# Kernel tuning notes

Hardware: AMD Instinct MI355X
Metric: run time of the kernel (lower is better)

The kernel has to match this reference:

```python
import jax, jax.numpy as jnp
import numpy as np

B, H, N, D = 4, 16, 2048, 64

def setup_inputs() -> dict:
    key = jax.random.key(0)
    kq, kk, kv = jax.random.split(key, 3)
    q = jax.random.normal(kq, (B, H, N, D), dtype=jnp.float32)
    k = jax.random.normal(kk, (B, H, N, D), dtype=jnp.float32)
    v = jax.random.normal(kv, (B, H, N, D), dtype=jnp.float32)
    return {"q": q, "k": k, "v": v}

def reference(q, k, v):
    head_dim = q.shape[-1]
    scale = 1.0 / jnp.sqrt(jnp.asarray(head_dim, dtype=q.dtype))
    # scores: [B, H, N, N]
    attn = jnp.einsum('bhqd,bhkd->bhqk', q, k) * scale
    attn = jax.nn.softmax(attn, axis=-1)
    # output: [B, H, N, D]
    return jnp.einsum('bhqk,bhkd->bhqd', attn, v)
```

## Files before the change

### kernel.cpp

```cpp
#include <hip/hip_runtime.h>
#include <hip/hip_bf16.h>
#include <math.h>

#define NBATCH 4
#define NHEAD 16
#define NSEQ 2048
#define DHEAD 64
#define QBLK 128
#define KVBLK 64
#define NTILE (NSEQ / KVBLK)
#define NHTOT (NBATCH * NHEAD)
#define KV_TILE_BYTES 16384
#define KVB_BYTES ((size_t)NHTOT * NTILE * (size_t)KV_TILE_BYTES)
#define WS_NEED KVB_BYTES
#define QSCALE (0.125f * 1.4426950408889634f)

typedef __attribute__((ext_vector_type(8))) short bf16x8;
typedef __attribute__((ext_vector_type(4))) short short4v;
typedef __attribute__((ext_vector_type(16))) float f32x16;

union BF8U { unsigned u[4]; bf16x8 v; };

__device__ __forceinline__ unsigned short f2bf(float f) {
  unsigned u = __float_as_uint(f);
  u = (u + 0x7FFFu + ((u >> 16) & 1u)) >> 16;
  return (unsigned short)u;
}
__device__ __forceinline__ unsigned pack2(float a, float b) {
  return (unsigned)f2bf(a) | ((unsigned)f2bf(b) << 16);
}
__device__ __forceinline__ unsigned cvtpk(float a, float b) {
  unsigned r;
  asm("v_cvt_pk_bf16_f32 %0, %1, %2" : "=v"(r) : "v"(a), "v"(b));
  return r;
}
__device__ __forceinline__ float exp2_fast(float x) {
#if __has_builtin(__builtin_amdgcn_exp2f)
  return __builtin_amdgcn_exp2f(x);
#else
  return __expf(x * 0.69314718055994531f);
#endif
}
__device__ __forceinline__ void gload_lds16(const void* g, void* l) {
  __builtin_amdgcn_global_load_lds(
      (const __attribute__((address_space(1))) void*)g,
      (__attribute__((address_space(3))) void*)l, 16, 0, 0);
}

__global__ __launch_bounds__(256) void prep_kernel(
    const float* __restrict__ K, const float* __restrict__ V,
    char* __restrict__ KVb) {
  __shared__ float vsm[64][68];
  const int t = threadIdx.x;
  const int hb = blockIdx.x;
  const int head = hb >> 5;
  const int tile = hb & 31;
  const float* kp = K + ((size_t)head * NSEQ + tile * KVBLK) * DHEAD;
  const float* vp = V + ((size_t)head * NSEQ + tile * KVBLK) * DHEAD;
  char* out = KVb + (size_t)hb * KV_TILE_BYTES;
#pragma unroll
  for (int j = 0; j < 2; ++j) {
    const int n = t + j * 256;
    const int key = n >> 3, ch = (n >> 1) & 3, hi = n & 1;
    const int d0 = ch * 16 + hi * 8;
    const float4 f0 = *(const float4*)(kp + key * DHEAD + d0);
    const float4 f1 = *(const float4*)(kp + key * DHEAD + d0 + 4);
    BF8U u;
    u.u[0] = cvtpk(f0.x, f0.y); u.u[1] = cvtpk(f0.z, f0.w);
    u.u[2] = cvtpk(f1.x, f1.y); u.u[3] = cvtpk(f1.z, f1.w);
    const int kk = key & 31;
    const int m2 = (kk >> 2) ^ ((kk & 3) << 1);
    const int off = ((key >> 5) << 12) | ((kk & 3) << 10) | (hi << 9) | (ch << 7) | (m2 << 4);
    *(bf16x8*)(out + off) = u.v;
  }
#pragma unroll
  for (int p = 0; p < 4; ++p) {
    const int key = (t & 15) + 16 * p;
    const int d0 = (t >> 4) * 4;
    *(float4*)(&vsm[key][d0]) = *(const float4*)(vp + key * DHEAD + d0);
  }
  __syncthreads();
#pragma unroll
  for (int j = 0; j < 2; ++j) {
    const int s = t + j * 256;
    const int aa = (s >> 4) & 3;
    const int sl = s & 7;
    const int d5 = ((sl ^ ((aa & 1) << 2)) << 2) | aa;
    const int khi = (s >> 3) & 1;
    const int c2 = (s >> 6) & 7;
    const int ch = c2 >> 1, dblk = c2 & 1;
    const int d = dblk * 32 + d5;
    const int k0 = ch * 16 + khi * 8;
    BF8U u;
    u.u[0] = cvtpk(vsm[k0 + 0][d], vsm[k0 + 1][d]);
    u.u[1] = cvtpk(vsm[k0 + 2][d], vsm[k0 + 3][d]);
    u.u[2] = cvtpk(vsm[k0 + 4][d], vsm[k0 + 5][d]);
    u.u[3] = cvtpk(vsm[k0 + 6][d], vsm[k0 + 7][d]);
    *(bf16x8*)(out + 8192 + (s << 4)) = u.v;
  }
}

__global__ __launch_bounds__(256, 3) void fattn_kernel(
    const float* __restrict__ Q, const char* __restrict__ KVb,
    float* __restrict__ O) {
  __shared__ __align__(128) char smem[4][8192];

  const int tid = threadIdx.x;
  const int l = tid & 63;
  const int wv = tid >> 6;
  const int l31 = l & 31;
  const int HL = l >> 5;

  const int head = blockIdx.x;
  const int q0 = blockIdx.y * QBLK + wv * 32;
  const size_t base = (size_t)head * NSEQ * DHEAD;

  bf16x8 qf[4];
  {
    const float* qrow = Q + base + (size_t)(q0 + l31) * DHEAD + HL * 8;
#pragma unroll
    for (int ch = 0; ch < 4; ++ch) {
      const float4 f0 = *(const float4*)(qrow + ch * 16);
      const float4 f1 = *(const float4*)(qrow + ch * 16 + 4);
      BF8U u;
      u.u[0] = cvtpk(f0.x * QSCALE, f0.y * QSCALE);
      u.u[1] = cvtpk(f0.z * QSCALE, f0.w * QSCALE);
      u.u[2] = cvtpk(f1.x * QSCALE, f1.y * QSCALE);
      u.u[3] = cvtpk(f1.z * QSCALE, f1.w * QSCALE);
      qf[ch] = u.v;
    }
  }

  const int kk = l31;
  const int m2x = (kk >> 2) ^ ((kk & 3) << 1);
  const int kread = ((kk & 3) << 10) + (HL << 9) + (m2x << 4);
  const int vsl = (l31 >> 2) ^ ((l & 1) << 2);
  const int vread = ((l & 3) << 8) + (HL << 7) + (vsl << 4);

  const char* tb = KVb + (size_t)head * NTILE * KV_TILE_BYTES;
  char* kb0 = smem[0]; char* kb1 = smem[1];
  char* vb0 = smem[2]; char* vb1 = smem[3];

#define STAGE_K(T, DST)                                                     \
  { const char* s_ = tb + (size_t)(T) * KV_TILE_BYTES;                      \
    gload_lds16(s_ + ((wv << 1) + 0) * 1024 + l * 16, (DST) + ((wv << 1) + 0) * 1024); \
    gload_lds16(s_ + ((wv << 1) + 1) * 1024 + l * 16, (DST) + ((wv << 1) + 1) * 1024); }
#define STAGE_V(T, DST)                                                     \
  { const char* s_ = tb + (size_t)(T) * KV_TILE_BYTES + 8192;               \
    gload_lds16(s_ + ((wv << 1) + 0) * 1024 + l * 16, (DST) + ((wv << 1) + 0) * 1024); \
    gload_lds16(s_ + ((wv << 1) + 1) * 1024 + l * 16, (DST) + ((wv << 1) + 1) * 1024); }

#define QK_MFMA(KB, D0, D1)                                                 \
  { const char* kbp_ = (const char*)(KB);                                   \
    { const bf16x8 ka0 = *(const bf16x8*)(kbp_ + kread);                    \
      const bf16x8 ka1 = *(const bf16x8*)(kbp_ + kread + 4096);             \
      D0 = __builtin_amdgcn_mfma_f32_32x32x16_bf16(ka0, qf[0], zz, 0, 0, 0);  \
      D1 = __builtin_amdgcn_mfma_f32_32x32x16_bf16(ka1, qf[0], zz, 0, 0, 0); } \
    _Pragma("unroll")                                                       \
    for (int ch = 1; ch < 4; ++ch) {                                        \
      const bf16x8 ka0 = *(const bf16x8*)(kbp_ + kread + ch * 128);         \
      const bf16x8 ka1 = *(const bf16x8*)(kbp_ + kread + ch * 128 + 4096);  \
      D0 = __builtin_amdgcn_mfma_f32_32x32x16_bf16(ka0, qf[ch], D0, 0, 0, 0); \
      D1 = __builtin_amdgcn_mfma_f32_32x32x16_bf16(ka1, qf[ch], D1, 0, 0, 0); \
    } }

#define SM_PACK(S0, S1, WREG)                                               \
  { _Pragma("unroll")                                                       \
    for (int r = 0; r < 16; ++r) { S0[r] = exp2_fast(S0[r]); S1[r] = exp2_fast(S1[r]); } \
    float bb[8];                                                            \
    _Pragma("unroll")                                                       \
    for (int i = 0; i < 8; ++i) bb[i] = (S0[i] + S0[i + 8]) + (S1[i] + S1[i + 8]); \
    _Pragma("unroll")                                                       \
    for (int i = 0; i < 4; ++i) bb[i] += bb[i + 4];                         \
    l_run += (bb[0] + bb[1]) + (bb[2] + bb[3]);                             \
    _Pragma("unroll")                                                       \
    for (int g = 0; g < 8; ++g) {                                           \
      WREG[0][g] = cvtpk(S0[2 * g], S0[2 * g + 1]);                         \
      WREG[1][g] = cvtpk(S1[2 * g], S1[2 * g + 1]);                         \
    } }

#define PV_MFMA(VB, WREG)                                                   \
  { const char* vbp_ = (const char*)(VB);                                   \
    _Pragma("unroll")                                                       \
    for (int ch = 0; ch < 4; ++ch) {                                        \
      const int sub = ch >> 1, e = ch & 1;                                  \
      unsigned a0 = WREG[sub][4 * e + 0], b0 = WREG[sub][4 * e + 2];        \
      unsigned a1 = WREG[sub][4 * e + 1], b1 = WREG[sub][4 * e + 3];        \
      asm("v_permlane32_swap_b32 %0, %1" : "+v"(a0), "+v"(b0));             \
      asm("v_permlane32_swap_b32 %0, %1" : "+v"(a1), "+v"(b1));             \
      BF8U pb;                                                              \
      pb.u[0] = a0; pb.u[1] = a1; pb.u[2] = b0; pb.u[3] = b1;               \
      const bf16x8 va0 = *(const bf16x8*)(vbp_ + vread + (ch * 2 + 0) * 1024); \
      const bf16x8 va1 = *(const bf16x8*)(vbp_ + vread + (ch * 2 + 1) * 1024); \
      o0 = __builtin_amdgcn_mfma_f32_32x32x16_bf16(va0, pb.v, o0, 0, 0, 0); \
      o1 = __builtin_amdgcn_mfma_f32_32x32x16_bf16(va1, pb.v, o1, 0, 0, 0); \
    } }

  f32x16 zz;
#pragma unroll
  for (int r = 0; r < 16; ++r) zz[r] = 0.f;
  f32x16 o0 = zz, o1 = zz;
  float l_run = 0.f;

  f32x16 sA0, sA1, sB0, sB1;

  STAGE_K(0, kb0);
  STAGE_V(0, vb0);
  STAGE_K(1, kb1);
  __syncthreads();
  QK_MFMA(kb0, sA0, sA1);
  __syncthreads();

  for (int t = 0; t < NTILE; t += 2) {
    if (t + 2 < NTILE) STAGE_K(t + 2, kb0);
    if (t + 1 < NTILE) STAGE_V(t + 1, vb1);
    QK_MFMA(kb1, sB0, sB1);
    {
      unsigned wreg[2][8];
      SM_PACK(sA0, sA1, wreg);
      PV_MFMA(vb0, wreg);
    }
    __syncthreads();

    if (t + 3 < NTILE) STAGE_K(t + 3, kb1);
    if (t + 2 < NTILE) STAGE_V(t + 2, vb0);
    if (t + 2 < NTILE) {
      QK_MFMA(kb0, sA0, sA1);
    }
    {
      unsigned wreg[2][8];
      SM_PACK(sB0, sB1, wreg);
      PV_MFMA(vb1, wreg);
    }
    __syncthreads();
  }

  l_run += __shfl_xor(l_run, 32);
  const float inv = 1.f / l_run;
  float* orow = O + base + (size_t)(q0 + l31) * DHEAD;
#pragma unroll
  for (int a2 = 0; a2 < 4; ++a2) {
    float4 v0, v1;
    v0.x = o0[4 * a2 + 0] * inv; v0.y = o0[4 * a2 + 1] * inv;
    v0.z = o0[4 * a2 + 2] * inv; v0.w = o0[4 * a2 + 3] * inv;
    *(float4*)(orow + 8 * a2 + 4 * HL) = v0;
    v1.x = o1[4 * a2 + 0] * inv; v1.y = o1[4 * a2 + 1] * inv;
    v1.z = o1[4 * a2 + 2] * inv; v1.w = o1[4 * a2 + 3] * inv;
    *(float4*)(orow + 8 * a2 + 4 * HL + 32) = v1;
  }
#undef STAGE_K
#undef STAGE_V
#undef QK_MFMA
#undef SM_PACK
#undef PV_MFMA
}

__global__ __launch_bounds__(256, 3) void fattn_fb(
    const float* __restrict__ Q, const float* __restrict__ K,
    const float* __restrict__ V, float* __restrict__ O) {
  __shared__ short klds[4096];
  __shared__ short vlds[4096];
  const int tid = threadIdx.x;
  const int l = tid & 63;
  const int wv = tid >> 6;
  const int l31 = l & 31;
  const int HL = l >> 5;
  const bool hib = (HL != 0);
  const int head = blockIdx.y;
  const size_t base = (size_t)head * NSEQ * DHEAD;
  const int q0 = blockIdx.x * 128 + wv * 32;
  bf16x8 qf[4];
  {
    const float* qrow = Q + base + (size_t)(q0 + l31) * DHEAD + HL * 8;
#pragma unroll
    for (int ch = 0; ch < 4; ++ch) {
      const float4 f0 = *(const float4*)(qrow + ch * 16);
      const float4 f1 = *(const float4*)(qrow + ch * 16 + 4);
      bf16x8 t;
      t[0] = (short)f2bf(f0.x * 0.125f); t[1] = (short)f2bf(f0.y * 0.125f);
      t[2] = (short)f2bf(f0.z * 0.125f); t[3] = (short)f2bf(f0.w * 0.125f);
      t[4] = (short)f2bf(f1.x * 0.125f); t[5] = (short)f2bf(f1.y * 0.125f);
      t[6] = (short)f2bf(f1.z * 0.125f); t[7] = (short)f2bf(f1.w * 0.125f);
      qf[ch] = t;
    }
  }
  const int skey_l = l & 15;
  const int sd0 = wv * 16 + ((l >> 4) & 3) * 4;
  const int kk = l31;
  const int m2x = (kk >> 2) ^ ((kk & 3) << 1);
  const int kread = ((kk & 3) << 10) + (HL << 9) + (m2x << 4);
  const int vread = ((l & 3) << 8) + (HL << 7) + ((l31 >> 2) << 4);
  char* kb = (char*)klds;
  char* vb = (char*)vlds;
  f32x16 o0, o1;
#pragma unroll
  for (int r = 0; r < 16; ++r) { o0[r] = 0.f; o1[r] = 0.f; }
  float m_run = -1e30f, l_run = 0.f;
  for (int it = 0; it < NTILE; ++it) {
    const int kv0 = it * KVBLK;
    __syncthreads();
#pragma unroll
    for (int p = 0; p < 4; ++p) {
      const int key = skey_l + 16 * p;
      const float4 kf = *(const float4*)(K + base + (size_t)(kv0 + key) * DHEAD + sd0);
      const float4 vf = *(const float4*)(V + base + (size_t)(kv0 + key) * DHEAD + sd0);
      const int kkw = key & 31;
      const int m2w = (kkw >> 2) ^ ((kkw & 3) << 1);
      const int koff = ((key >> 5) << 12) + ((kkw & 3) << 10) + (((sd0 >> 3) & 1) << 9)
                     + ((sd0 >> 4) << 7) + (m2w << 4) + ((sd0 & 7) << 1);
      short4v kb4;
      kb4[0] = (short)f2bf(kf.x); kb4[1] = (short)f2bf(kf.y);
      kb4[2] = (short)f2bf(kf.z); kb4[3] = (short)f2bf(kf.w);
      *(short4v*)(kb + koff) = kb4;
      const int vbase2 = ((p * 2 + (sd0 >> 5)) << 10) + (((key >> 3) & 1) << 7)
                       + (((sd0 & 31) >> 2) << 4) + ((key & 7) << 1);
      *(short*)(vb + vbase2 + 0)   = (short)f2bf(vf.x);
      *(short*)(vb + vbase2 + 256) = (short)f2bf(vf.y);
      *(short*)(vb + vbase2 + 512) = (short)f2bf(vf.z);
      *(short*)(vb + vbase2 + 768) = (short)f2bf(vf.w);
    }
    __syncthreads();
    f32x16 s0, s1;
#pragma unroll
    for (int r = 0; r < 16; ++r) { s0[r] = 0.f; s1[r] = 0.f; }
#pragma unroll
    for (int ch = 0; ch < 4; ++ch) {
      const bf16x8 ka0 = *(const bf16x8*)(kb + kread + ch * 128);
      const bf16x8 ka1 = *(const bf16x8*)(kb + kread + ch * 128 + 4096);
      s0 = __builtin_amdgcn_mfma_f32_32x32x16_bf16(ka0, qf[ch], s0, 0, 0, 0);
      s1 = __builtin_amdgcn_mfma_f32_32x32x16_bf16(ka1, qf[ch], s1, 0, 0, 0);
    }
    float mx = s0[0];
#pragma unroll
    for (int r = 1; r < 16; ++r) mx = fmaxf(mx, s0[r]);
#pragma unroll
    for (int r = 0; r < 16; ++r) mx = fmaxf(mx, s1[r]);
    mx = fmaxf(mx, __shfl_xor(mx, 32));
    const float m_new = fmaxf(m_run, mx);
    const float alpha = __expf(m_run - m_new);
    m_run = m_new;
    float rsum = 0.f;
#pragma unroll
    for (int r = 0; r < 16; ++r) { s0[r] = __expf(s0[r] - m_new); rsum += s0[r]; }
#pragma unroll
    for (int r = 0; r < 16; ++r) { s1[r] = __expf(s1[r] - m_new); rsum += s1[r]; }
    rsum += __shfl_xor(rsum, 32);
    l_run = l_run * alpha + rsum;
    o0 *= alpha;
    o1 *= alpha;
    unsigned wreg[2][8], xreg[2][8];
#pragma unroll
    for (int g = 0; g < 8; ++g) {
      wreg[0][g] = pack2(s0[2 * g], s0[2 * g + 1]);
      wreg[1][g] = pack2(s1[2 * g], s1[2 * g + 1]);
    }
#pragma unroll
    for (int sub = 0; sub < 2; ++sub)
#pragma unroll
      for (int g = 0; g < 8; ++g)
        xreg[sub][g] = (unsigned)__shfl_xor((int)wreg[sub][g], 32);
#pragma unroll
    for (int ch = 0; ch < 4; ++ch) {
      const int sub = ch >> 1, e = ch & 1;
      const unsigned lo0 = hib ? xreg[sub][4 * e + 2] : wreg[sub][4 * e + 0];
      const unsigned lo1 = hib ? xreg[sub][4 * e + 3] : wreg[sub][4 * e + 1];
      const unsigned hi0 = hib ? wreg[sub][4 * e + 2] : xreg[sub][4 * e + 0];
      const unsigned hi1 = hib ? wreg[sub][4 * e + 3] : xreg[sub][4 * e + 1];
      BF8U pb;
      pb.u[0] = lo0; pb.u[1] = lo1; pb.u[2] = hi0; pb.u[3] = hi1;
      const bf16x8 va0 = *(const bf16x8*)(vb + vread + (ch * 2 + 0) * 1024);
      const bf16x8 va1 = *(const bf16x8*)(vb + vread + (ch * 2 + 1) * 1024);
      o0 = __builtin_amdgcn_mfma_f32_32x32x16_bf16(va0, pb.v, o0, 0, 0, 0);
      o1 = __builtin_amdgcn_mfma_f32_32x32x16_bf16(va1, pb.v, o1, 0, 0, 0);
    }
  }
  const float inv = 1.f / l_run;
  float* orow = O + base + (size_t)(q0 + l31) * DHEAD;
#pragma unroll
  for (int a = 0; a < 4; ++a) {
    float4 v0, v1;
    v0.x = o0[4 * a + 0] * inv; v0.y = o0[4 * a + 1] * inv;
    v0.z = o0[4 * a + 2] * inv; v0.w = o0[4 * a + 3] * inv;
    *(float4*)(orow + 8 * a + 4 * HL) = v0;
    v1.x = o1[4 * a + 0] * inv; v1.y = o1[4 * a + 1] * inv;
    v1.z = o1[4 * a + 2] * inv; v1.w = o1[4 * a + 3] * inv;
    *(float4*)(orow + 8 * a + 4 * HL + 32) = v1;
  }
}

extern "C" void kernel_launch(void* const* d_in, const int* in_sizes, int n_in,
                              void* d_out, int out_size, void* d_ws, size_t ws_size,
                              hipStream_t stream) {
  const float* q = (const float*)d_in[0];
  const float* k = (const float*)d_in[1];
  const float* v = (const float*)d_in[2];
  float* o = (float*)d_out;
  if (ws_size < WS_NEED) {
    dim3 grid(NSEQ / 128, NHTOT, 1);
    fattn_fb<<<grid, dim3(256, 1, 1), 0, stream>>>(q, k, v, o);
    return;
  }
  char* KVb = (char*)d_ws;
  prep_kernel<<<dim3(NHTOT * NTILE, 1, 1), dim3(256, 1, 1), 0, stream>>>(k, v, KVb);
  dim3 grid(NHTOT, NSEQ / QBLK, 1);
  fattn_kernel<<<grid, dim3(256, 1, 1), 0, stream>>>(q, KVb, o);
}
```

Baseline: 100.0 us.

## Load V fragments directly from global into registers, skipping LDS staging

```diff
diff --git a/kernel.cpp b/kernel.cpp
--- a/kernel.cpp
+++ b/kernel.cpp
@@ -103,7 +103,7 @@
 __global__ __launch_bounds__(256, 3) void fattn_kernel(
     const float* __restrict__ Q, const char* __restrict__ KVb,
     float* __restrict__ O) {
-  __shared__ __align__(128) char smem[4][8192];
+  __shared__ __align__(128) char smem[2][8192];
 
   const int tid = threadIdx.x;
   const int l = tid & 63;
@@ -135,20 +135,22 @@
   const int m2x = (kk >> 2) ^ ((kk & 3) << 1);
   const int kread = ((kk & 3) << 10) + (HL << 9) + (m2x << 4);
   const int vsl = (l31 >> 2) ^ ((l & 1) << 2);
-  const int vread = ((l & 3) << 8) + (HL << 7) + (vsl << 4);
+  const int vread = 8192 + ((l & 3) << 8) + (HL << 7) + (vsl << 4);
 
   const char* tb = KVb + (size_t)head * NTILE * KV_TILE_BYTES;
+  const char* vgbase = tb + vread;
   char* kb0 = smem[0]; char* kb1 = smem[1];
-  char* vb0 = smem[2]; char* vb1 = smem[3];
 
 #define STAGE_K(T, DST)                                                     \
   { const char* s_ = tb + (size_t)(T) * KV_TILE_BYTES;                      \
     gload_lds16(s_ + ((wv << 1) + 0) * 1024 + l * 16, (DST) + ((wv << 1) + 0) * 1024); \
     gload_lds16(s_ + ((wv << 1) + 1) * 1024 + l * 16, (DST) + ((wv << 1) + 1) * 1024); }
-#define STAGE_V(T, DST)                                                     \
-  { const char* s_ = tb + (size_t)(T) * KV_TILE_BYTES + 8192;               \
-    gload_lds16(s_ + ((wv << 1) + 0) * 1024 + l * 16, (DST) + ((wv << 1) + 0) * 1024); \
-    gload_lds16(s_ + ((wv << 1) + 1) * 1024 + l * 16, (DST) + ((wv << 1) + 1) * 1024); }
+
+#define LOAD_V(T)                                                           \
+  { const char* vp_ = vgbase + (size_t)(T) * KV_TILE_BYTES;                 \
+    _Pragma("unroll")                                                       \
+    for (int c2 = 0; c2 < 8; ++c2)                                          \
+      va[c2] = *(const bf16x8*)(vp_ + c2 * 1024); }
 
 #define QK_MFMA(KB, D0, D1)                                                 \
   { const char* kbp_ = (const char*)(KB);                                   \
@@ -179,9 +181,8 @@
       WREG[1][g] = cvtpk(S1[2 * g], S1[2 * g + 1]);                         \
     } }
 
-#define PV_MFMA(VB, WREG)                                                   \
-  { const char* vbp_ = (const char*)(VB);                                   \
-    _Pragma("unroll")                                                       \
+#define PV_MFMA(WREG)                                                       \
+  { _Pragma("unroll")                                                       \
     for (int ch = 0; ch < 4; ++ch) {                                        \
       const int sub = ch >> 1, e = ch & 1;                                  \
       unsigned a0 = WREG[sub][4 * e + 0], b0 = WREG[sub][4 * e + 2];        \
@@ -190,10 +191,8 @@
       asm("v_permlane32_swap_b32 %0, %1" : "+v"(a1), "+v"(b1));             \
       BF8U pb;                                                              \
       pb.u[0] = a0; pb.u[1] = a1; pb.u[2] = b0; pb.u[3] = b1;               \
-      const bf16x8 va0 = *(const bf16x8*)(vbp_ + vread + (ch * 2 + 0) * 1024); \
-      const bf16x8 va1 = *(const bf16x8*)(vbp_ + vread + (ch * 2 + 1) * 1024); \
-      o0 = __builtin_amdgcn_mfma_f32_32x32x16_bf16(va0, pb.v, o0, 0, 0, 0); \
-      o1 = __builtin_amdgcn_mfma_f32_32x32x16_bf16(va1, pb.v, o1, 0, 0, 0); \
+      o0 = __builtin_amdgcn_mfma_f32_32x32x16_bf16(va[ch * 2 + 0], pb.v, o0, 0, 0, 0); \
+      o1 = __builtin_amdgcn_mfma_f32_32x32x16_bf16(va[ch * 2 + 1], pb.v, o1, 0, 0, 0); \
     } }
 
   f32x16 zz;
@@ -203,9 +202,9 @@
   float l_run = 0.f;
 
   f32x16 sA0, sA1, sB0, sB1;
+  bf16x8 va[8];
 
   STAGE_K(0, kb0);
-  STAGE_V(0, vb0);
   STAGE_K(1, kb1);
   __syncthreads();
   QK_MFMA(kb0, sA0, sA1);
@@ -213,24 +212,24 @@
 
   for (int t = 0; t < NTILE; t += 2) {
     if (t + 2 < NTILE) STAGE_K(t + 2, kb0);
-    if (t + 1 < NTILE) STAGE_V(t + 1, vb1);
+    LOAD_V(t);
     QK_MFMA(kb1, sB0, sB1);
     {
       unsigned wreg[2][8];
       SM_PACK(sA0, sA1, wreg);
-      PV_MFMA(vb0, wreg);
+      PV_MFMA(wreg);
     }
     __syncthreads();
 
     if (t + 3 < NTILE) STAGE_K(t + 3, kb1);
-    if (t + 2 < NTILE) STAGE_V(t + 2, vb0);
+    LOAD_V(t + 1);
     if (t + 2 < NTILE) {
       QK_MFMA(kb0, sA0, sA1);
     }
     {
       unsigned wreg[2][8];
       SM_PACK(sB0, sB1, wreg);
-      PV_MFMA(vb1, wreg);
+      PV_MFMA(wreg);
     }
     __syncthreads();
   }
@@ -249,7 +248,7 @@
     *(float4*)(orow + 8 * a2 + 4 * HL + 32) = v1;
   }
 #undef STAGE_K
-#undef STAGE_V
+#undef LOAD_V
 #undef QK_MFMA
 #undef SM_PACK
 #undef PV_MFMA
```

Result: slower. 190.5 us (+90.5%).
